# Performance work log

Measured on AMD Instinct MI355X. Metric: run time of the kernel, lower is better.

Reference implementation:

```python
import jax, jax.numpy as jnp
import numpy as np

N = 100000
E = 1600000
IN_C = 128
HEADS = 4
HEAD_D = 32  # out_channels(128) // heads(4)


def setup_inputs() -> dict:
    key = jax.random.key(0)
    k1, k2, k3, k4, k5, k6 = jax.random.split(key, 6)
    x = jax.random.normal(k1, (N, IN_C), dtype=jnp.float32)
    edge_index = jax.random.randint(k2, (2, E), 0, N, dtype=jnp.int64)
    edge_weight = jax.random.uniform(k3, (E,), dtype=jnp.float32)
    # params: linear weight stored as [in, H*D] so forward is x @ W (torch does x @ weight.T)
    W = jax.random.normal(k4, (IN_C, HEADS * HEAD_D), dtype=jnp.float32) * (1.0 / np.sqrt(IN_C))
    att_src = jax.random.normal(k5, (HEADS, HEAD_D), dtype=jnp.float32) * 0.1
    att_dst = jax.random.normal(k6, (HEADS, HEAD_D), dtype=jnp.float32) * 0.1
    return {"x": x, "W": W, "att_src": att_src, "att_dst": att_dst,
            "edge_weight": edge_weight, "edge_index": edge_index, "num_nodes": N}


def reference(x, W, att_src, att_dst, edge_weight, edge_index, num_nodes):
    H, D = att_src.shape
    xw = (x @ W).reshape(-1, H, D)                       # [N, H, D]
    row, col = edge_index[0], edge_index[1]
    a_src = jnp.einsum('nhd,hd->nh', xw, att_src)        # [N, H]
    a_dst = jnp.einsum('nhd,hd->nh', xw, att_dst)        # [N, H]
    alpha = jax.nn.leaky_relu(a_src[row] + a_dst[col], negative_slope=0.2)  # [E, H]
    # segment softmax over edges grouped by row (destination of aggregation)
    amax = jax.ops.segment_max(alpha, row, num_segments=num_nodes)          # [N, H]
    amax = jnp.where(jnp.isfinite(amax), amax, 0.0)      # empty segments -> 0 (matches torch init)
    alpha = jnp.exp(alpha - amax[row])
    asum = jax.ops.segment_sum(alpha, row, num_segments=num_nodes)          # [N, H]
    alpha = alpha / (asum[row] + 1e-16)
    msg = xw[col] * alpha[..., None]                     # [E, H, D]
    out = jax.ops.segment_sum(msg, row, num_segments=num_nodes)             # [N, H, D]
    return out.reshape(num_nodes, H * D)
```

## Files before the change

### kernel.cpp

```cpp
#include <hip/hip_runtime.h>
#include <math.h>


typedef _Float16 half4 __attribute__((ext_vector_type(4)));
typedef _Float16 half8 __attribute__((ext_vector_type(8)));
typedef float    f32x4 __attribute__((ext_vector_type(4)));

#define PCHUNK   4096
#define NB_SHIFT 8
#define BCAP     4864
#define GTILES   8

__device__ __forceinline__ float lrelu_exp(float v) {
    return __expf(fmaxf(v, 0.2f * v));
}

__global__ __launch_bounds__(128) void k_prep(const float* __restrict__ W,
                                              const float* __restrict__ att_src,
                                              const float* __restrict__ att_dst,
                                              _Float16* __restrict__ Wa) {
    int n = blockIdx.x;
    int k = threadIdx.x;
    float v;
    if (n < 128) {
        v = W[(size_t)k * 128 + n];
    } else if (n < 136) {
        int h = (n - 128) & 3;
        const float* att = (n < 132) ? att_src : att_dst;
        float s = 0.f;
        #pragma unroll
        for (int d = 0; d < 32; ++d)
            s += W[(size_t)k * 128 + h * 32 + d] * att[h * 32 + d];
        v = s;
    } else {
        v = 0.f;
    }
    Wa[n * 128 + k] = (_Float16)v;
}

__device__ __forceinline__ _Float16* lds_ptr(_Float16* base, int r, int kf16) {
    int g = (kf16 >> 3) ^ (r & 7);
    return base + r * 128 + g * 8 + (kf16 & 7);
}

__global__ __launch_bounds__(256) void k_fat(const float* __restrict__ x,
                                             const _Float16* __restrict__ Wa,
                                             _Float16* __restrict__ xwh,
                                             float* __restrict__ a_src,
                                             float* __restrict__ a_dst, int N,
                                             const int* __restrict__ eidx,
                                             int* __restrict__ bctr,
                                             unsigned* __restrict__ rec, int E,
                                             int nPart) {
    __shared__ __align__(16) char smem[57360];
    int bid = blockIdx.x;
    int t = threadIdx.x;
    int lane = t & 63, wv = t >> 6;

    if (bid < nPart) {
        unsigned long long* buf = (unsigned long long*)smem;
        unsigned* sbuf = (unsigned*)(smem + 32768);
        int* hist = (int*)(smem + 49152);
        int* excl = hist + 512;
        int* gbase = excl + 512;
        int* cur = gbase + 512;
        int* wtot = cur + 512;
        int e0 = bid * PCHUNK;
        int nE = E - e0; if (nE > PCHUNK) nE = PCHUNK;
        hist[t] = 0; hist[t + 256] = 0;
        __syncthreads();
        for (int i = t; i < nE; i += 256) {
            int row = __builtin_nontemporal_load(&eidx[e0 + i]);
            int col = __builtin_nontemporal_load(&eidx[E + e0 + i]);
            buf[i] = ((unsigned long long)(unsigned)col << 32) | (unsigned)row;
            atomicAdd(&hist[row >> NB_SHIFT], 1);
        }
        __syncthreads();
        int h0 = hist[2 * t], h1 = hist[2 * t + 1];
        int s = h0 + h1, sc = s;
        #pragma unroll
        for (int off = 1; off < 64; off <<= 1) {
            int v = __shfl_up(sc, off);
            if (lane >= off) sc += v;
        }
        if (lane == 63) wtot[wv] = sc;
        __syncthreads();
        if (t == 0) {
            int run = 0;
            #pragma unroll
            for (int i = 0; i < 4; ++i) { int tmp = wtot[i]; wtot[i] = run; run += tmp; }
        }
        __syncthreads();
        int incl = sc + wtot[wv];
        excl[2 * t]     = incl - s;
        excl[2 * t + 1] = incl - h1;
        cur[2 * t]      = incl - s;
        cur[2 * t + 1]  = incl - h1;
        gbase[2 * t]     = h0 ? atomicAdd(&bctr[2 * t], h0) : 0;
        gbase[2 * t + 1] = h1 ? atomicAdd(&bctr[2 * t + 1], h1) : 0;
        __syncthreads();
        unsigned long long myrec[PCHUNK / 256];
        #pragma unroll
        for (int k = 0; k < PCHUNK / 256; ++k) {
            int i = t + k * 256;
            if (i < nE) myrec[k] = buf[i];
        }
        __syncthreads();
        unsigned short* bkt16 = (unsigned short*)buf;
        #pragma unroll
        for (int k = 0; k < PCHUNK / 256; ++k) {
            int i = t + k * 256;
            if (i < nE) {
                unsigned long long rr = myrec[k];
                int row = (int)(unsigned)rr;
                int b = row >> NB_SHIFT;
                int dst = atomicAdd(&cur[b], 1);
                sbuf[dst] = ((unsigned)(rr >> 32) << 8) | ((unsigned)row & 255u);
                bkt16[dst] = (unsigned short)b;
            }
        }
        __syncthreads();
        for (int j = t; j < nE; j += 256) {
            unsigned rr = sbuf[j];
            int b = bkt16[j];
            int off = gbase[b] + (j - excl[b]);
            if (off < BCAP)
                __builtin_nontemporal_store(rr, &rec[(size_t)b * BCAP + off]);
        }
        return;
    }

    int gid = bid - nPart;
    _Float16* Xs = (_Float16*)smem;
    _Float16* Ws = (_Float16*)(smem + 16384);
    int lm = lane & 15, lg = lane >> 4;
    int brow0 = gid * (64 * GTILES);
    int ntiles = (N - brow0 + 63) >> 6;
    if (ntiles > GTILES) ntiles = GTILES;

    #pragma unroll
    for (int i = 0; i < 9; ++i) {
        int f = (i * 256 + t) * 8;
        int nr = f >> 7, kc = f & 127;
        *(half8*)lds_ptr(Ws, nr, kc) = *(const half8*)&Wa[f];
    }

    int srow[4], skc[4];
    #pragma unroll
    for (int i = 0; i < 4; ++i) {
        int f = (i * 256 + t) * 8;
        srow[i] = f >> 7;
        skc[i]  = f & 127;
    }
    float4 xr0[4], xr1[4];
    #pragma unroll
    for (int i = 0; i < 4; ++i) {
        int gr = brow0 + srow[i]; if (gr >= N) gr = N - 1;
        xr0[i] = *(const float4*)&x[(size_t)gr * 128 + skc[i]];
        xr1[i] = *(const float4*)&x[(size_t)gr * 128 + skc[i] + 4];
    }

    for (int g = 0; g < ntiles; ++g) {
        int row0 = brow0 + g * 64;
        __syncthreads();
        #pragma unroll
        for (int i = 0; i < 4; ++i) {
            half8 hv;
            hv[0] = (_Float16)xr0[i].x; hv[1] = (_Float16)xr0[i].y;
            hv[2] = (_Float16)xr0[i].z; hv[3] = (_Float16)xr0[i].w;
            hv[4] = (_Float16)xr1[i].x; hv[5] = (_Float16)xr1[i].y;
            hv[6] = (_Float16)xr1[i].z; hv[7] = (_Float16)xr1[i].w;
            *(half8*)lds_ptr(Xs, srow[i], skc[i]) = hv;
        }
        __syncthreads();
        if (g + 1 < ntiles) {
            #pragma unroll
            for (int i = 0; i < 4; ++i) {
                int gr = row0 + 64 + srow[i]; if (gr >= N) gr = N - 1;
                xr0[i] = *(const float4*)&x[(size_t)gr * 128 + skc[i]];
                xr1[i] = *(const float4*)&x[(size_t)gr * 128 + skc[i] + 4];
            }
        }
        f32x4 acc[9];
        #pragma unroll
        for (int nn = 0; nn < 9; ++nn) acc[nn] = (f32x4){0.f, 0.f, 0.f, 0.f};
        #pragma unroll
        for (int kk = 0; kk < 4; ++kk) {
            int kb = kk * 32 + lg * 8;
            half8 a0 = *(const half8*)lds_ptr(Xs, wv * 16 + lm, kb);
            #pragma unroll
            for (int nn = 0; nn < 9; ++nn) {
                half8 b = *(const half8*)lds_ptr(Ws, nn * 16 + lm, kb);
                acc[nn] = __builtin_amdgcn_mfma_f32_16x16x32_f16(a0, b, acc[nn], 0, 0, 0);
            }
        }
        #pragma unroll
        for (int reg = 0; reg < 4; ++reg) {
            int row = row0 + wv * 16 + lg * 4 + reg;
            if (row < N) {
                #pragma unroll
                for (int nn = 0; nn < 8; ++nn)
                    xwh[(size_t)row * 128 + nn * 16 + lm] = (_Float16)acc[nn][reg];
                float lv = acc[8][reg];
                if (lm < 4)      a_src[(size_t)row * 4 + lm]       = lv;
                else if (lm < 8) a_dst[(size_t)row * 4 + (lm - 4)] = lv;
            }
        }
    }
}

__global__ __launch_bounds__(256) void k_csr(const unsigned* __restrict__ rec,
                                             const int* __restrict__ bctr,
                                             int2* __restrict__ rseg,
                                             int* __restrict__ csr_col, int N) {
    __shared__ int cnt[256], cur[256];
    __shared__ int wtot[4];
    int b = blockIdx.x;
    int rs = b << NB_SHIFT;
    int t = threadIdx.x;
    int lane = t & 63, wv = t >> 6;
    cnt[t] = 0;
    __syncthreads();
    int m = bctr[b]; if (m > BCAP) m = BCAP;
    const unsigned* rr = &rec[(size_t)b * BCAP];
    for (int i = t; i < m; i += 256) {
        unsigned r = rr[i];
        atomicAdd(&cnt[r & 255u], 1);
    }
    __syncthreads();
    int c = cnt[t], sc = c;
    #pragma unroll
    for (int off = 1; off < 64; off <<= 1) {
        int v = __shfl_up(sc, off);
        if (lane >= off) sc += v;
    }
    if (lane == 63) wtot[wv] = sc;
    __syncthreads();
    if (t == 0) {
        int run = 0;
        #pragma unroll
        for (int i = 0; i < 4; ++i) { int tmp = wtot[i]; wtot[i] = run; run += tmp; }
    }
    __syncthreads();
    int ex = sc + wtot[wv] - c;
    cur[t] = ex;
    int n = rs + t;
    if (n < N) {
        int2 sg;
        sg.x = b * BCAP + ex;
        sg.y = b * BCAP + ex + c;
        rseg[n] = sg;
    }
    __syncthreads();
    for (int i = t; i < m; i += 256) {
        unsigned r = rr[i];
        int slot = atomicAdd(&cur[r & 255u], 1);
        csr_col[b * BCAP + slot] = (int)(r >> 8);
    }
}

__global__ __launch_bounds__(256) void k_agg(const int2* __restrict__ rseg,
                                             const int* __restrict__ csr_col,
                                             const float* __restrict__ a_src,
                                             const float* __restrict__ a_dst,
                                             const _Float16* __restrict__ xwh,
                                             float* __restrict__ out,
                                             int n0, int n1) {
    int lane = threadIdx.x & 63;
    int n = n0 + blockIdx.x * 4 + (threadIdx.x >> 6);
    if (n >= n1) return;
    int2 seg = rseg[n];
    int beg = seg.x, end = seg.y;
    int q = lane >> 4;
    int l = lane & 15;
    int h = l >> 2;
    float s_n = a_src[(size_t)n * 4 + h];
    float acc[8] = {0, 0, 0, 0, 0, 0, 0, 0};
    float ws = 0.f;

    for (int w0 = beg; w0 < end; w0 += 64) {
        int rem = end - w0; if (rem > 64) rem = 64;
        int cc = (lane < rem) ? __builtin_nontemporal_load(&csr_col[w0 + lane]) : 0;
        int j = 0;
        for (; j + 16 <= rem; j += 16) {
            int c[4]; float ad[4]; half8 xv[4];
            #pragma unroll
            for (int u = 0; u < 4; ++u) c[u] = __shfl(cc, j + u * 4 + q);
            #pragma unroll
            for (int u = 0; u < 4; ++u) {
                ad[u] = a_dst[(size_t)c[u] * 4 + h];
                xv[u] = *(const half8*)&xwh[(size_t)c[u] * 128 + (l << 3)];
            }
            #pragma unroll
            for (int u = 0; u < 4; ++u) {
                float w = lrelu_exp(s_n + ad[u]);
                ws += w;
                #pragma unroll
                for (int k = 0; k < 8; ++k)
                    acc[k] += w * (float)xv[u][k];
            }
        }
        if (j < rem) {
            int c[4]; float m[4]; float ad[4]; half8 xv[4];
            #pragma unroll
            for (int u = 0; u < 4; ++u) {
                int r = j + u * 4 + q;
                c[u] = __shfl(cc, r);
                m[u] = (r < rem) ? 1.f : 0.f;
            }
            #pragma unroll
            for (int u = 0; u < 4; ++u) {
                ad[u] = a_dst[(size_t)c[u] * 4 + h];
                xv[u] = *(const half8*)&xwh[(size_t)c[u] * 128 + (l << 3)];
            }
            #pragma unroll
            for (int u = 0; u < 4; ++u) {
                float w = m[u] * lrelu_exp(s_n + ad[u]);
                ws += w;
                #pragma unroll
                for (int k = 0; k < 8; ++k)
                    acc[k] += w * (float)xv[u][k];
            }
        }
    }

    #pragma unroll
    for (int k = 0; k < 8; ++k) {
        acc[k] += __shfl_xor(acc[k], 16);
        acc[k] += __shfl_xor(acc[k], 32);
    }
    ws += __shfl_xor(ws, 16);
    ws += __shfl_xor(ws, 32);
    if (q == 0) {
        float inv = 1.0f / (ws + 1e-16f);
        f32x4 o0 = {acc[0] * inv, acc[1] * inv, acc[2] * inv, acc[3] * inv};
        f32x4 o1 = {acc[4] * inv, acc[5] * inv, acc[6] * inv, acc[7] * inv};
        __builtin_nontemporal_store(o0, (f32x4*)&out[(size_t)n * 128 + (l << 3)]);
        __builtin_nontemporal_store(o1, (f32x4*)&out[(size_t)n * 128 + (l << 3) + 4]);
    }
}

extern "C" void kernel_launch(void* const* d_in, const int* in_sizes, int n_in,
                              void* d_out, int out_size, void* d_ws, size_t ws_size,
                              hipStream_t stream) {
    const float* x       = (const float*)d_in[0];
    const float* W       = (const float*)d_in[1];
    const float* att_src = (const float*)d_in[2];
    const float* att_dst = (const float*)d_in[3];
    const int* eidx      = (const int*)d_in[5];
    int N = in_sizes[0] / 128;
    int E = in_sizes[4];
    float* out = (float*)d_out;

    char* p = (char*)d_ws;
    auto alloc = [&](size_t bytes) {
        char* r = p;
        p += (bytes + 255) & ~(size_t)255;
        return r;
    };
    int nbuckets = (N + 255) >> NB_SHIFT;
    _Float16* xwh  = (_Float16*)alloc((size_t)N * 128 * 2);
    float* a_src   = (float*)alloc((size_t)N * 4 * 4);
    float* a_dst   = (float*)alloc((size_t)N * 4 * 4);
    int*   bctr    = (int*)  alloc(512 * 4);
    unsigned* rec  = (unsigned*)alloc((size_t)nbuckets * BCAP * 4);
    int2*  rseg    = (int2*) alloc((size_t)N * 8);
    int*   csr_col = (int*)  alloc((size_t)nbuckets * BCAP * 4);
    _Float16* Wa   = (_Float16*)alloc(144 * 128 * 2);

    int nPart  = (E + PCHUNK - 1) / PCHUNK;
    int nGemmB = (N + 64 * GTILES - 1) / (64 * GTILES);

    (void)hipMemsetAsync(bctr, 0, 512 * 4, stream);
    k_prep<<<144, 128, 0, stream>>>(W, att_src, att_dst, Wa);
    k_fat<<<nPart + nGemmB, 256, 0, stream>>>(x, Wa, xwh, a_src, a_dst, N,
                                              eidx, bctr, rec, E, nPart);
    k_csr<<<nbuckets, 256, 0, stream>>>(rec, bctr, rseg, csr_col, N);
    int third = N / 3;
    k_agg<<<(third + 3) / 4, 256, 0, stream>>>(rseg, csr_col, a_src, a_dst, xwh, out, 0, third);
    k_agg<<<(third + 3) / 4, 256, 0, stream>>>(rseg, csr_col, a_src, a_dst, xwh, out, third, 2 * third);
    k_agg<<<(N - 2 * third + 3) / 4, 256, 0, stream>>>(rseg, csr_col, a_src, a_dst, xwh, out, 2 * third, N);
}
```

Before: 251.4 us.

## Split fused partition/GEMM kernel into separate launches and fold bctr reset into prep

The fused k_fat kernel, which ran edge partitioning and the x@W MFMA GEMM in different blocks of one launch, is split into k_gemm and k_part. Each now gets its own shared-memory footprint, which can raise occupancy. PCHUNK and GTILES are halved to launch more, smaller blocks. The bucket counter memset moves into k_prep, which drops one memset launch, and the aggregation is split into two launches instead of three. The cost is serializing two phases that previously overlapped inside one launch.

```diff
diff --git a/kernel.cpp b/kernel.cpp
--- a/kernel.cpp
+++ b/kernel.cpp
@@ -6,10 +6,10 @@
 typedef _Float16 half8 __attribute__((ext_vector_type(8)));
 typedef float    f32x4 __attribute__((ext_vector_type(4)));
 
-#define PCHUNK   4096
+#define PCHUNK   2048
 #define NB_SHIFT 8
 #define BCAP     4864
-#define GTILES   8
+#define GTILES   4
 
 __device__ __forceinline__ float lrelu_exp(float v) {
     return __expf(fmaxf(v, 0.2f * v));
@@ -18,9 +18,14 @@
 __global__ __launch_bounds__(128) void k_prep(const float* __restrict__ W,
                                               const float* __restrict__ att_src,
                                               const float* __restrict__ att_dst,
-                                              _Float16* __restrict__ Wa) {
+                                              _Float16* __restrict__ Wa,
+                                              int* __restrict__ bctr) {
     int n = blockIdx.x;
     int k = threadIdx.x;
+    if (n == 0) {
+        #pragma unroll
+        for (int i = 0; i < 4; ++i) bctr[k * 4 + i] = 0;
+    }
     float v;
     if (n < 128) {
         v = W[(size_t)k * 128 + n];
@@ -43,98 +48,17 @@
     return base + r * 128 + g * 8 + (kf16 & 7);
 }
 
-__global__ __launch_bounds__(256) void k_fat(const float* __restrict__ x,
-                                             const _Float16* __restrict__ Wa,
-                                             _Float16* __restrict__ xwh,
-                                             float* __restrict__ a_src,
-                                             float* __restrict__ a_dst, int N,
-                                             const int* __restrict__ eidx,
-                                             int* __restrict__ bctr,
-                                             unsigned* __restrict__ rec, int E,
-                                             int nPart) {
-    __shared__ __align__(16) char smem[57360];
-    int bid = blockIdx.x;
+__global__ __launch_bounds__(256) void k_gemm(const float* __restrict__ x,
+                                              const _Float16* __restrict__ Wa,
+                                              _Float16* __restrict__ xwh,
+                                              float* __restrict__ a_src,
+                                              float* __restrict__ a_dst, int N) {
+    __shared__ _Float16 Xs[64 * 128];
+    __shared__ _Float16 Ws[144 * 128];
     int t = threadIdx.x;
     int lane = t & 63, wv = t >> 6;
-
-    if (bid < nPart) {
-        unsigned long long* buf = (unsigned long long*)smem;
-        unsigned* sbuf = (unsigned*)(smem + 32768);
-        int* hist = (int*)(smem + 49152);
-        int* excl = hist + 512;
-        int* gbase = excl + 512;
-        int* cur = gbase + 512;
-        int* wtot = cur + 512;
-        int e0 = bid * PCHUNK;
-        int nE = E - e0; if (nE > PCHUNK) nE = PCHUNK;
-        hist[t] = 0; hist[t + 256] = 0;
-        __syncthreads();
-        for (int i = t; i < nE; i += 256) {
-            int row = __builtin_nontemporal_load(&eidx[e0 + i]);
-            int col = __builtin_nontemporal_load(&eidx[E + e0 + i]);
-            buf[i] = ((unsigned long long)(unsigned)col << 32) | (unsigned)row;
-            atomicAdd(&hist[row >> NB_SHIFT], 1);
-        }
-        __syncthreads();
-        int h0 = hist[2 * t], h1 = hist[2 * t + 1];
-        int s = h0 + h1, sc = s;
-        #pragma unroll
-        for (int off = 1; off < 64; off <<= 1) {
-            int v = __shfl_up(sc, off);
-            if (lane >= off) sc += v;
-        }
-        if (lane == 63) wtot[wv] = sc;
-        __syncthreads();
-        if (t == 0) {
-            int run = 0;
-            #pragma unroll
-            for (int i = 0; i < 4; ++i) { int tmp = wtot[i]; wtot[i] = run; run += tmp; }
-        }
-        __syncthreads();
-        int incl = sc + wtot[wv];
-        excl[2 * t]     = incl - s;
-        excl[2 * t + 1] = incl - h1;
-        cur[2 * t]      = incl - s;
-        cur[2 * t + 1]  = incl - h1;
-        gbase[2 * t]     = h0 ? atomicAdd(&bctr[2 * t], h0) : 0;
-        gbase[2 * t + 1] = h1 ? atomicAdd(&bctr[2 * t + 1], h1) : 0;
-        __syncthreads();
-        unsigned long long myrec[PCHUNK / 256];
-        #pragma unroll
-        for (int k = 0; k < PCHUNK / 256; ++k) {
-            int i = t + k * 256;
-            if (i < nE) myrec[k] = buf[i];
-        }
-        __syncthreads();
-        unsigned short* bkt16 = (unsigned short*)buf;
-        #pragma unroll
-        for (int k = 0; k < PCHUNK / 256; ++k) {
-            int i = t + k * 256;
-            if (i < nE) {
-                unsigned long long rr = myrec[k];
-                int row = (int)(unsigned)rr;
-                int b = row >> NB_SHIFT;
-                int dst = atomicAdd(&cur[b], 1);
-                sbuf[dst] = ((unsigned)(rr >> 32) << 8) | ((unsigned)row & 255u);
-                bkt16[dst] = (unsigned short)b;
-            }
-        }
-        __syncthreads();
-        for (int j = t; j < nE; j += 256) {
-            unsigned rr = sbuf[j];
-            int b = bkt16[j];
-            int off = gbase[b] + (j - excl[b]);
-            if (off < BCAP)
-                __builtin_nontemporal_store(rr, &rec[(size_t)b * BCAP + off]);
-        }
-        return;
-    }
-
-    int gid = bid - nPart;
-    _Float16* Xs = (_Float16*)smem;
-    _Float16* Ws = (_Float16*)(smem + 16384);
     int lm = lane & 15, lg = lane >> 4;
-    int brow0 = gid * (64 * GTILES);
+    int brow0 = blockIdx.x * (64 * GTILES);
     int ntiles = (N - brow0 + 63) >> 6;
     if (ntiles > GTILES) ntiles = GTILES;
 
@@ -206,6 +130,82 @@
                 else if (lm < 8) a_dst[(size_t)row * 4 + (lm - 4)] = lv;
             }
         }
+    }
+}
+
+__global__ __launch_bounds__(256) void k_part(const int* __restrict__ eidx,
+                                              int* __restrict__ bctr,
+                                              unsigned* __restrict__ rec,
+                                              int E) {
+    __shared__ unsigned long long buf[PCHUNK];
+    __shared__ unsigned sbuf[PCHUNK];
+    __shared__ int hist[512];
+    __shared__ int gbase[512], cur[512];
+    __shared__ int wtot[4];
+    int t = threadIdx.x;
+    int lane = t & 63, wv = t >> 6;
+    int e0 = blockIdx.x * PCHUNK;
+    int nE = E - e0; if (nE > PCHUNK) nE = PCHUNK;
+    hist[t] = 0; hist[t + 256] = 0;
+    __syncthreads();
+    for (int i = t; i < nE; i += 256) {
+        int row = __builtin_nontemporal_load(&eidx[e0 + i]);
+        int col = __builtin_nontemporal_load(&eidx[E + e0 + i]);
+        buf[i] = ((unsigned long long)(unsigned)col << 32) | (unsigned)row;
+        atomicAdd(&hist[row >> NB_SHIFT], 1);
+    }
+    __syncthreads();
+    int h0 = hist[2 * t], h1 = hist[2 * t + 1];
+    int s = h0 + h1, sc = s;
+    #pragma unroll
+    for (int off = 1; off < 64; off <<= 1) {
+        int v = __shfl_up(sc, off);
+        if (lane >= off) sc += v;
+    }
+    if (lane == 63) wtot[wv] = sc;
+    __syncthreads();
+    if (t == 0) {
+        int run = 0;
+        #pragma unroll
+        for (int i = 0; i < 4; ++i) { int tmp = wtot[i]; wtot[i] = run; run += tmp; }
+    }
+    __syncthreads();
+    int incl = sc + wtot[wv];
+    int* excl = hist;
+    excl[2 * t]     = incl - s;
+    excl[2 * t + 1] = incl - h1;
+    cur[2 * t]      = incl - s;
+    cur[2 * t + 1]  = incl - h1;
+    gbase[2 * t]     = h0 ? atomicAdd(&bctr[2 * t], h0) : 0;
+    gbase[2 * t + 1] = h1 ? atomicAdd(&bctr[2 * t + 1], h1) : 0;
+    __syncthreads();
+    unsigned long long myrec[PCHUNK / 256];
+    #pragma unroll
+    for (int k = 0; k < PCHUNK / 256; ++k) {
+        int i = t + k * 256;
+        if (i < nE) myrec[k] = buf[i];
+    }
+    __syncthreads();
+    unsigned short* bkt16 = (unsigned short*)buf;
+    #pragma unroll
+    for (int k = 0; k < PCHUNK / 256; ++k) {
+        int i = t + k * 256;
+        if (i < nE) {
+            unsigned long long rr = myrec[k];
+            int row = (int)(unsigned)rr;
+            int b = row >> NB_SHIFT;
+            int dst = atomicAdd(&cur[b], 1);
+            sbuf[dst] = ((unsigned)(rr >> 32) << 8) | ((unsigned)row & 255u);
+            bkt16[dst] = (unsigned short)b;
+        }
+    }
+    __syncthreads();
+    for (int j = t; j < nE; j += 256) {
+        unsigned rr = sbuf[j];
+        int b = bkt16[j];
+        int off = gbase[b] + (j - excl[b]);
+        if (off < BCAP)
+            __builtin_nontemporal_store(rr, &rec[(size_t)b * BCAP + off]);
     }
 }
 
@@ -368,16 +368,11 @@
     int*   csr_col = (int*)  alloc((size_t)nbuckets * BCAP * 4);
     _Float16* Wa   = (_Float16*)alloc(144 * 128 * 2);
 
-    int nPart  = (E + PCHUNK - 1) / PCHUNK;
-    int nGemmB = (N + 64 * GTILES - 1) / (64 * GTILES);
-
-    (void)hipMemsetAsync(bctr, 0, 512 * 4, stream);
-    k_prep<<<144, 128, 0, stream>>>(W, att_src, att_dst, Wa);
-    k_fat<<<nPart + nGemmB, 256, 0, stream>>>(x, Wa, xwh, a_src, a_dst, N,
-                                              eidx, bctr, rec, E, nPart);
+    k_prep<<<144, 128, 0, stream>>>(W, att_src, att_dst, Wa, bctr);
+    k_gemm<<<(N + 64 * GTILES - 1) / (64 * GTILES), 256, 0, stream>>>(x, Wa, xwh, a_src, a_dst, N);
+    k_part<<<(E + PCHUNK - 1) / PCHUNK, 256, 0, stream>>>(eidx, bctr, rec, E);
     k_csr<<<nbuckets, 256, 0, stream>>>(rec, bctr, rseg, csr_col, N);
-    int third = N / 3;
-    k_agg<<<(third + 3) / 4, 256, 0, stream>>>(rseg, csr_col, a_src, a_dst, xwh, out, 0, third);
-    k_agg<<<(third + 3) / 4, 256, 0, stream>>>(rseg, csr_col, a_src, a_dst, xwh, out, third, 2 * third);
-    k_agg<<<(N - 2 * third + 3) / 4, 256, 0, stream>>>(rseg, csr_col, a_src, a_dst, xwh, out, 2 * third, N);
-}
+    int half = N / 2;
+    k_agg<<<(half + 3) / 4, 256, 0, stream>>>(rseg, csr_col, a_src, a_dst, xwh, out, 0, half);
+    k_agg<<<(N - half + 3) / 4, 256, 0, stream>>>(rseg, csr_col, a_src, a_dst, xwh, out, half, N);
+}
```

New measurement: 252.8 us. Within noise of the previous version (+0.5%).
